# Performance work log

Hardware: AMD Instinct MI355X
Metric: run time of the kernel (lower is better)

## Reference

```python
import jax, jax.numpy as jnp
import numpy as np

S = 0.1          # slab half-width: |sum(y)| <= S
R2 = 0.02        # ball radius squared: ||y||^2 <= R2
EPS = 1e-12


def _project(z):
    """Euclidean projection of each row of z onto {y : |1^T y|<=S, ||y||^2<=R2}.

    KKT case analysis:
      1) project onto slab only; accept if inside ball
      2) project onto ball only; accept if inside slab
      3) both constraints active: y = c*z + ((sign(t)*S - c*t)/n)*1 with
         c = sqrt((n*R2 - S^2) / (n*||z||^2 - t^2)),  t = 1^T z.
    """
    n = z.shape[-1]
    t = jnp.sum(z, axis=-1, keepdims=True)                       # [B,1]
    zz = jnp.sum(z * z, axis=-1, keepdims=True)                  # [B,1]

    # case 1: slab projection (contains z itself when already feasible)
    y1 = z + (jnp.clip(t, -S, S) - t) / n
    ok1 = jnp.sum(y1 * y1, axis=-1, keepdims=True) <= R2

    # case 2: ball projection
    znorm = jnp.sqrt(jnp.maximum(zz, EPS))
    scale = jnp.minimum(1.0, jnp.sqrt(R2) / znorm)
    y2 = z * scale
    ok2 = jnp.abs(t) * scale <= S

    # case 3: both active
    denom = jnp.maximum(n * zz - t * t, EPS)                     # >= 0 by Cauchy-Schwarz
    c = jnp.sqrt(jnp.maximum(n * R2 - S * S, 0.0) / denom)
    sp = jnp.sign(t) * S
    y3 = c * z + (sp - c * t) / n

    return jnp.where(ok1, y1, jnp.where(ok2, y2, y3))


def setup_inputs() -> dict:
    key = jax.random.key(0)
    k1, k2, k3 = jax.random.split(key, 3)
    B, D_in, D_out = 65536, 512, 256
    x = jax.random.normal(k1, (B, D_in), dtype=jnp.float32)
    # params (scaled so z = W@x - b straddles the feasible region boundary)
    W = 0.01 * jax.random.normal(k2, (D_out, D_in), dtype=jnp.float32)
    b = 0.01 * jax.random.normal(k3, (D_out,), dtype=jnp.float32)
    return {"x": x, "W": W, "b": b}


def reference(x, W, b):
    z = x @ W.T - b                                              # [B, D_out]
    return _project(z)
```

## Files before the change

### kernel.cpp

```cpp
#include <hip/hip_runtime.h>


typedef __bf16 bf16x8 __attribute__((ext_vector_type(8)));
typedef float f32x4 __attribute__((ext_vector_type(4)));

#define BM 128
#define BN 256
#define BK 64
#define THREADS 512

__device__ __forceinline__ unsigned short f2bf(float f) {
    unsigned u = __builtin_bit_cast(unsigned, f);
    u += 0x7fffu + ((u >> 16) & 1u);
    return (unsigned short)(u >> 16);
}

__global__ void wconv_kernel(const float* __restrict__ W,
                             unsigned short* __restrict__ Wb) {
    int i = (blockIdx.x * 256 + threadIdx.x) * 4;
    float4 v = *(const float4*)(W + i);
    ushort4 h;
    h.x = f2bf(v.x); h.y = f2bf(v.y); h.z = f2bf(v.z); h.w = f2bf(v.w);
    *(ushort4*)(Wb + i) = h;
}

__global__ __launch_bounds__(THREADS, 4)
void proj_gemm_kernel(const float* __restrict__ x,
                      const unsigned short* __restrict__ Wb,
                      const float* __restrict__ b,
                      float* __restrict__ out) {
    __shared__ alignas(16) unsigned short Abuf[BM * BK];
    __shared__ alignas(16) unsigned short Bbuf[2][BN * BK];

    const int tid  = threadIdx.x;
    const int lane = tid & 63;
    const int wv   = tid >> 6;
    const int wm   = wv >> 2;
    const int wn   = wv & 3;
    const int ln   = lane & 15;
    const int quad = lane >> 4;
    const int m0   = blockIdx.x * BM;

    const int arow = tid >> 4;
    const int kq   = tid & 15;
    const float* xbase = x + (long)(m0 + arow) * 512 + kq * 4;

    unsigned awb[4];
    #pragma unroll
    for (int p = 0; p < 4; ++p) {
        const int row = arow + p * 32;
        awb[p] = (unsigned)((row * 128 + kq * 8) ^ ((row & 7) << 4));
    }

    const int b_r0 = wv * 32 + (lane >> 3);
    const int b_cg = (lane & 7) ^ (lane >> 3);

    f32x4 acc[4][4];
    #pragma unroll
    for (int mi = 0; mi < 4; ++mi)
        #pragma unroll
        for (int ni = 0; ni < 4; ++ni)
            acc[mi][ni] = (f32x4){0.f, 0.f, 0.f, 0.f};

    float4 areg[4];

    auto issue_B = [&](int kt, int buf) {
        const int k0 = kt * BK;
        #pragma unroll
        for (int j = 0; j < 4; ++j) {
            const unsigned short* src =
                Wb + (long)(b_r0 + j * 8) * 512 + k0 + b_cg * 8;
            __builtin_amdgcn_global_load_lds(
                (const __attribute__((address_space(1))) void*)src,
                (__attribute__((address_space(3))) void*)(unsigned long)(unsigned int)
                    (unsigned long)(uintptr_t)&Bbuf[buf][(wv * 4 + j) * 512],
                16, 0, 0);
        }
    };
    auto load_A = [&](int kt) {
        const int k0 = kt * BK;
        #pragma unroll
        for (int p = 0; p < 4; ++p)
            areg[p] = *(const float4*)(xbase + (long)p * 32 * 512 + k0);
    };
    auto write_A = [&]() {
        #pragma unroll
        for (int p = 0; p < 4; ++p) {
            ushort4 h;
            h.x = f2bf(areg[p].x); h.y = f2bf(areg[p].y);
            h.z = f2bf(areg[p].z); h.w = f2bf(areg[p].w);
            *(ushort4*)((char*)Abuf + awb[p]) = h;
        }
    };

    issue_B(0, 0);
    load_A(0);

    for (int kt = 0; kt < 8; ++kt) {
        const int cur = kt & 1;
        if (kt < 7) {
            issue_B(kt + 1, cur ^ 1);
            asm volatile("s_waitcnt vmcnt(4)" ::: "memory");
        } else {
            asm volatile("s_waitcnt vmcnt(0)" ::: "memory");
        }
        write_A();
        if (kt < 7) load_A(kt + 1);
        asm volatile("s_waitcnt lgkmcnt(0)" ::: "memory");
        __builtin_amdgcn_s_barrier();

        #pragma unroll
        for (int ks = 0; ks < 2; ++ks) {
            bf16x8 bf[4];
            #pragma unroll
            for (int ni = 0; ni < 4; ++ni) {
                const int r  = wn * 64 + ni * 16 + ln;
                const int cc = (ks * 4 + quad) ^ (ln & 7);
                bf[ni] = *(const bf16x8*)&Bbuf[cur][r * 64 + cc * 8];
            }
            #pragma unroll
            for (int mi = 0; mi < 4; ++mi) {
                const int row = wm * 64 + mi * 16 + ln;
                const unsigned arb =
                    (unsigned)(row * 128 + ((((ks << 2) | quad) ^ (ln & 7)) << 4));
                bf16x8 af = *(const bf16x8*)((const char*)Abuf + arb);
                #pragma unroll
                for (int ni = 0; ni < 4; ++ni)
                    acc[mi][ni] = __builtin_amdgcn_mfma_f32_16x16x32_bf16(
                        af, bf[ni], acc[mi][ni], 0, 0, 0);
            }
        }
        asm volatile("s_waitcnt lgkmcnt(0)" ::: "memory");
        __builtin_amdgcn_s_barrier();
    }

    float bb[4];
    #pragma unroll
    for (int ni = 0; ni < 4; ++ni) bb[ni] = b[wn * 64 + ni * 16 + ln];
    #pragma unroll
    for (int mi = 0; mi < 4; ++mi)
        #pragma unroll
        for (int ni = 0; ni < 4; ++ni)
            #pragma unroll
            for (int r = 0; r < 4; ++r)
                acc[mi][ni][r] -= bb[ni];

    __syncthreads();
    float* P  = (float*)Abuf;
    float* AB = P + 128 * 8;

    #pragma unroll
    for (int mi = 0; mi < 4; ++mi) {
        #pragma unroll
        for (int r = 0; r < 4; ++r) {
            float s1 = 0.f, s2 = 0.f;
            #pragma unroll
            for (int ni = 0; ni < 4; ++ni) {
                float v = acc[mi][ni][r];
                s1 += v; s2 += v * v;
            }
            #pragma unroll
            for (int off = 1; off < 16; off <<= 1) {
                s1 += __shfl_xor(s1, off, 64);
                s2 += __shfl_xor(s2, off, 64);
            }
            if (ln == 0) {
                int row = wm * 64 + mi * 16 + quad * 4 + r;
                P[row * 8 + wn * 2 + 0] = s1;
                P[row * 8 + wn * 2 + 1] = s2;
            }
        }
    }
    __syncthreads();

    if (tid < 128) {
        int row = tid;
        float t  = P[row*8+0] + P[row*8+2] + P[row*8+4] + P[row*8+6];
        float zz = P[row*8+1] + P[row*8+3] + P[row*8+5] + P[row*8+7];
        const float S = 0.1f, R2 = 0.02f, nf = 256.f, inv_n = 1.f / 256.f;
        float tc    = fminf(fmaxf(t, -S), S);
        float beta1 = (tc - t) * inv_n;
        float ny1   = zz + 2.f * beta1 * t + nf * beta1 * beta1;
        float alpha, beta;
        if (ny1 <= R2) {
            alpha = 1.f; beta = beta1;
        } else {
            float znorm = sqrtf(fmaxf(zz, 1e-12f));
            float scale = fminf(1.f, 0.14142135623730951f / znorm);
            if (fabsf(t) * scale <= S) {
                alpha = scale; beta = 0.f;
            } else {
                float denom = fmaxf(nf * zz - t * t, 1e-12f);
                float c  = sqrtf(5.11f / denom);
                float sp = (t > 0.f) ? S : ((t < 0.f) ? -S : 0.f);
                alpha = c; beta = (sp - c * t) * inv_n;
            }
        }
        AB[row*2+0] = alpha;
        AB[row*2+1] = beta;
    }
    __syncthreads();

    #pragma unroll
    for (int mi = 0; mi < 4; ++mi) {
        #pragma unroll
        for (int r = 0; r < 4; ++r) {
            int row = wm * 64 + mi * 16 + quad * 4 + r;
            float alpha = AB[row*2+0];
            float beta  = AB[row*2+1];
            float* orow = out + (long)(m0 + row) * 256 + wn * 64 + ln;
            #pragma unroll
            for (int ni = 0; ni < 4; ++ni)
                orow[ni*16] = alpha * acc[mi][ni][r] + beta;
        }
    }
}

extern "C" void kernel_launch(void* const* d_in, const int* in_sizes, int n_in,
                              void* d_out, int out_size, void* d_ws, size_t ws_size,
                              hipStream_t stream) {
    const float* x = (const float*)d_in[0];
    const float* W = (const float*)d_in[1];
    const float* b = (const float*)d_in[2];
    float* out = (float*)d_out;
    unsigned short* Wb = (unsigned short*)d_ws;

    const int Dout = in_sizes[2];
    const int Din  = in_sizes[1] / Dout;
    const int Btot = in_sizes[0] / Din;

    wconv_kernel<<<(Dout * Din) / (256 * 4), 256, 0, stream>>>(W, Wb);
    proj_gemm_kernel<<<Btot / BM, THREADS, 0, stream>>>(x, Wb, b, out);
}
```

Before: 220.9 us.

## Read W fragments directly from global/L2 and double-buffer the A tile

Drops the LDS staging of the bf16 weight tile and has each wave load its B fragments straight from global memory, relying on the small 256 KB weight matrix staying in cache. A is now double-buffered in LDS, so the next tile is written after the MFMA loop and there is one barrier per k-step instead of two. This frees a lot of shared memory, which can raise occupancy. The cost is that each wave makes redundant global loads of W whose latency is exposed just before the MFMAs, with no prefetch.

```diff
diff --git a/kernel.cpp b/kernel.cpp
--- a/kernel.cpp
+++ b/kernel.cpp
@@ -29,8 +29,7 @@
                       const unsigned short* __restrict__ Wb,
                       const float* __restrict__ b,
                       float* __restrict__ out) {
-    __shared__ alignas(16) unsigned short Abuf[BM * BK];
-    __shared__ alignas(16) unsigned short Bbuf[2][BN * BK];
+    __shared__ alignas(16) unsigned short Abuf[2][BM * BK];
 
     const int tid  = threadIdx.x;
     const int lane = tid & 63;
@@ -52,9 +51,6 @@
         awb[p] = (unsigned)((row * 128 + kq * 8) ^ ((row & 7) << 4));
     }
 
-    const int b_r0 = wv * 32 + (lane >> 3);
-    const int b_cg = (lane & 7) ^ (lane >> 3);
-
     f32x4 acc[4][4];
     #pragma unroll
     for (int mi = 0; mi < 4; ++mi)
@@ -64,74 +60,54 @@
 
     float4 areg[4];
 
-    auto issue_B = [&](int kt, int buf) {
-        const int k0 = kt * BK;
-        #pragma unroll
-        for (int j = 0; j < 4; ++j) {
-            const unsigned short* src =
-                Wb + (long)(b_r0 + j * 8) * 512 + k0 + b_cg * 8;
-            __builtin_amdgcn_global_load_lds(
-                (const __attribute__((address_space(1))) void*)src,
-                (__attribute__((address_space(3))) void*)(unsigned long)(unsigned int)
-                    (unsigned long)(uintptr_t)&Bbuf[buf][(wv * 4 + j) * 512],
-                16, 0, 0);
-        }
-    };
     auto load_A = [&](int kt) {
         const int k0 = kt * BK;
         #pragma unroll
         for (int p = 0; p < 4; ++p)
             areg[p] = *(const float4*)(xbase + (long)p * 32 * 512 + k0);
     };
-    auto write_A = [&]() {
+    auto write_A = [&](int buf) {
         #pragma unroll
         for (int p = 0; p < 4; ++p) {
             ushort4 h;
             h.x = f2bf(areg[p].x); h.y = f2bf(areg[p].y);
             h.z = f2bf(areg[p].z); h.w = f2bf(areg[p].w);
-            *(ushort4*)((char*)Abuf + awb[p]) = h;
+            *(ushort4*)((char*)Abuf[buf] + awb[p]) = h;
         }
     };
 
-    issue_B(0, 0);
     load_A(0);
+    write_A(0);
+    __syncthreads();
 
     for (int kt = 0; kt < 8; ++kt) {
         const int cur = kt & 1;
-        if (kt < 7) {
-            issue_B(kt + 1, cur ^ 1);
-            asm volatile("s_waitcnt vmcnt(4)" ::: "memory");
-        } else {
-            asm volatile("s_waitcnt vmcnt(0)" ::: "memory");
-        }
-        write_A();
         if (kt < 7) load_A(kt + 1);
-        asm volatile("s_waitcnt lgkmcnt(0)" ::: "memory");
-        __builtin_amdgcn_s_barrier();
-
+
+        const int k0 = kt * BK;
         #pragma unroll
         for (int ks = 0; ks < 2; ++ks) {
             bf16x8 bf[4];
             #pragma unroll
             for (int ni = 0; ni < 4; ++ni) {
-                const int r  = wn * 64 + ni * 16 + ln;
-                const int cc = (ks * 4 + quad) ^ (ln & 7);
-                bf[ni] = *(const bf16x8*)&Bbuf[cur][r * 64 + cc * 8];
+                const int r = wn * 64 + ni * 16 + ln;
+                bf[ni] = *(const bf16x8*)(Wb + (long)r * 512 + k0 + ks * 32 + quad * 8);
             }
             #pragma unroll
             for (int mi = 0; mi < 4; ++mi) {
                 const int row = wm * 64 + mi * 16 + ln;
                 const unsigned arb =
                     (unsigned)(row * 128 + ((((ks << 2) | quad) ^ (ln & 7)) << 4));
-                bf16x8 af = *(const bf16x8*)((const char*)Abuf + arb);
+                bf16x8 af = *(const bf16x8*)((const char*)Abuf[cur] + arb);
                 #pragma unroll
                 for (int ni = 0; ni < 4; ++ni)
                     acc[mi][ni] = __builtin_amdgcn_mfma_f32_16x16x32_bf16(
                         af, bf[ni], acc[mi][ni], 0, 0, 0);
             }
         }
-        asm volatile("s_waitcnt lgkmcnt(0)" ::: "memory");
-        __builtin_amdgcn_s_barrier();
+
+        if (kt < 7) write_A(cur ^ 1);
+        __syncthreads();
     }
 
     float bb[4];
@@ -145,8 +121,7 @@
             for (int r = 0; r < 4; ++r)
                 acc[mi][ni][r] -= bb[ni];
 
-    __syncthreads();
-    float* P  = (float*)Abuf;
+    float* P  = (float*)&Abuf[0][0];
     float* AB = P + 128 * 8;
 
     #pragma unroll
```

After: 235.4 us. +6.5%, slower.
